# Kernel optimization log

Measured on AMD Instinct MI355X. Metric: run time of the kernel, lower is better.

The kernel has to match this reference:

```python
import jax, jax.numpy as jnp
import numpy as np

N_IN = 500000
N_OUT = 125000
K = 8          # kernel^dim = 2^3 offsets
R = 62500      # rulebook pairs per offset (strided conv: total == N_IN)
RS = 62500     # submanifold rulebook pairs per offset
C_IN = 64
C_OUT = 128
BN_EPS = 1e-4  # scn.BatchNormReLU default eps


def bn_relu(x, gamma, beta):
    # SCN BatchNormReLU in training mode: per-channel stats over active sites.
    m = jnp.mean(x, axis=0)
    v = jnp.var(x, axis=0)
    return jax.nn.relu((x - m) * jax.lax.rsqrt(v + BN_EPS) * gamma + beta)


def sparse_conv(x, W, in_idx, out_idx, n_out):
    # rulebook gather-GEMM-scatter.
    # x: [N_in, Cin]; W: [K, Cin, Cout]; in_idx/out_idx: [K, R]
    g = x[in_idx]                                   # [K, R, Cin] gather
    c = jnp.einsum('krc,kcd->krd', g, W)            # per-offset GEMM
    out = jnp.zeros((n_out, W.shape[-1]), x.dtype)
    return out.at[out_idx.reshape(-1)].add(c.reshape(-1, W.shape[-1]))


def setup_inputs() -> dict:
    key = jax.random.key(0)
    ks = jax.random.split(key, 8)
    x = jax.random.normal(ks[0], (N_IN, C_IN), dtype=jnp.float32)
    W1 = jax.random.normal(ks[1], (K, C_IN, C_OUT), dtype=jnp.float32) / np.sqrt(K * C_IN)
    Ws = jax.random.normal(ks[2], (K, C_OUT, C_OUT), dtype=jnp.float32) / np.sqrt(K * C_OUT)
    W2 = jax.random.normal(ks[3], (K, C_IN, C_OUT), dtype=jnp.float32) / np.sqrt(K * C_IN)
    in_idx1 = jax.random.randint(ks[4], (K, R), 0, N_IN, dtype=jnp.int32)
    out_idx1 = jax.random.randint(ks[5], (K, R), 0, N_OUT, dtype=jnp.int32)
    in_idx_s = jax.random.randint(ks[6], (K, RS), 0, N_OUT, dtype=jnp.int32)
    out_idx_s = jax.random.randint(ks[7], (K, RS), 0, N_OUT, dtype=jnp.int32)
    return {
        'x': x,
        'gamma1': jnp.ones((C_IN,), jnp.float32),
        'beta1': jnp.zeros((C_IN,), jnp.float32),
        'gamma2': jnp.ones((C_OUT,), jnp.float32),
        'beta2': jnp.zeros((C_OUT,), jnp.float32),
        'W1': W1, 'Ws': Ws, 'W2': W2,
        'in_idx1': in_idx1, 'out_idx1': out_idx1,
        'in_idx_s': in_idx_s, 'out_idx_s': out_idx_s,
        'n_out': N_OUT,
    }


def reference(x, gamma1, beta1, gamma2, beta2, W1, Ws, W2,
              in_idx1, out_idx1, in_idx_s, out_idx_s, n_out):
    x1 = bn_relu(x, gamma1, beta1)                              # bnr1
    y1 = sparse_conv(x1, W1, in_idx1, out_idx1, n_out)          # conv1 (stride 2)
    y1 = bn_relu(y1, gamma2, beta2)                             # bnr2
    y1 = sparse_conv(y1, Ws, in_idx_s, out_idx_s, n_out)        # submanifold conv
    y2 = sparse_conv(x1, W2, in_idx1, out_idx1, n_out)          # conv2 (same rulebook)
    return y1 + y2                                              # AddTable
```

## Files before the change

kernel.cpp:

```cpp
#include <hip/hip_runtime.h>

#define K_OFF   8
#define R_PAIRS 62500
#define NPAIRS  500000
#define N_IN    500000
#define N_OUT   125000
#define CIN     64
#define COUT    128
#define BN_EPS  1e-4f
#define NBINS_KC (N_OUT * K_OFF)
#define NB2     (2 * NBINS_KC)
#define SCAN_E2 8192
#define NSB2    245
#define BM      32
#define CHUNK   32
#define OLD_TILES 8

typedef __bf16 bf16;
typedef __bf16 bf16x4 __attribute__((ext_vector_type(4)));
typedef __bf16 bf16x8 __attribute__((ext_vector_type(8)));
typedef float  f32x4  __attribute__((ext_vector_type(4)));
typedef unsigned int u32;

__device__ __forceinline__ int zb(int row, int col_bf16) {
    int byte = (row << 10) + (col_bf16 << 1);
    return byte ^ ((row & 7) << 4);
}

template<int C>
__global__ void bn_stats_kernel(const float* __restrict__ x, int n_rows,
                                float* __restrict__ sums ) {
    constexpr int CG = C / 4;
    int tid = blockIdx.x * blockDim.x + threadIdx.x;
    int nth = gridDim.x * blockDim.x;
    const float4* x4 = (const float4*)x;
    long n4 = (long)n_rows * CG;
    int cg = tid % CG;
    float s[4] = {0,0,0,0}, q[4] = {0,0,0,0};
    for (long i = tid; i < n4; i += nth) {
        float4 v = x4[i];
        float f[4] = {v.x, v.y, v.z, v.w};
        #pragma unroll
        for (int j = 0; j < 4; j++) { s[j] += f[j]; q[j] += f[j] * f[j]; }
    }
    __shared__ float acc[2 * C];
    for (int i = threadIdx.x; i < 2 * C; i += blockDim.x) acc[i] = 0.f;
    __syncthreads();
    #pragma unroll
    for (int j = 0; j < 4; j++) {
        atomicAdd(&acc[cg * 4 + j], s[j]);
        atomicAdd(&acc[C + cg * 4 + j], q[j]);
    }
    __syncthreads();
    for (int i = threadIdx.x; i < 2 * C; i += blockDim.x) atomicAdd(&sums[i], acc[i]);
}

template<int C>
__global__ void bn_finalize_kernel(const float* __restrict__ sums,
                                   const float* __restrict__ gamma,
                                   const float* __restrict__ beta,
                                   float inv_n, float* __restrict__ ss) {
    int c = threadIdx.x;
    if (c < C) {
        float m  = sums[c] * inv_n;
        float v  = sums[C + c] * inv_n - m * m;
        float sc = gamma[c] * rsqrtf(v + BN_EPS);
        ss[c]     = sc;
        ss[C + c] = beta[c] - m * sc;
    }
}

__global__ void bn_finalize2_kernel(const float* __restrict__ S ,
                                    const float* __restrict__ gamma,
                                    const float* __restrict__ beta,
                                    float* __restrict__ ss) {
    int c = threadIdx.x;
    float s = 0.f, q = 0.f;
    for (int st = 0; st < 64; st++) { s += S[st * 256 + c]; q += S[st * 256 + 128 + c]; }
    float m = s / (float)N_OUT;
    float v = q / (float)N_OUT - m * m;
    float sc = gamma[c] * rsqrtf(v + BN_EPS);
    ss[c] = sc; ss[128 + c] = beta[c] - m * sc;
}

__global__ void pack12_kernel(const float* __restrict__ W1, const float* __restrict__ W2,
                              bf16* __restrict__ Wf) {
    int idx = blockIdx.x * 256 + threadIdx.x;
    int j = idx & 7;
    int lane = (idx >> 3) & 63;
    int fi = idx >> 9;
    int ks = fi >> 4, nfrag = fi & 15;
    int k512 = ks * 32 + (lane >> 4) * 8 + j;
    int koff = k512 >> 6, kc = k512 & 63;
    int c = nfrag * 16 + (lane & 15);
    const float* W = (c < 128) ? W1 : W2;
    Wf[idx] = (bf16)W[((long)koff * CIN + kc) * COUT + (c & 127)];
}

__global__ void packS_kernel(const float* __restrict__ Ws, bf16* __restrict__ Wf) {
    int idx = blockIdx.x * 256 + threadIdx.x;
    int j = idx & 7;
    int lane = (idx >> 3) & 63;
    int fi = idx >> 9;
    int ksg = fi >> 3, nfrag = fi & 7;
    int k1024 = ksg * 32 + (lane >> 4) * 8 + j;
    int koff = k1024 >> 7, kc = k1024 & 127;
    int c = nfrag * 16 + (lane & 15);
    Wf[idx] = (bf16)Ws[((long)koff * COUT + kc) * COUT + c];
}

__global__ void hist2_kernel(const int* __restrict__ o1, const int* __restrict__ os,
                             u32* __restrict__ counts) {
    int p = blockIdx.x * blockDim.x + threadIdx.x;
    int stride = gridDim.x * blockDim.x;
    for (; p < 2 * NPAIRS; p += stride) {
        int bin;
        if (p < NPAIRS) bin = o1[p] * K_OFF + p / R_PAIRS;
        else { int q = p - NPAIRS; bin = NBINS_KC + os[q] * K_OFF + q / R_PAIRS; }
        atomicAdd(&counts[bin], 1u);
    }
}

__global__ void scan1_kernel(const u32* __restrict__ counts, u32* __restrict__ bsum, int n) {
    __shared__ u32 sd[256];
    int tid = threadIdx.x;
    int base = blockIdx.x * SCAN_E2 + tid * 32;
    u32 s = 0;
    #pragma unroll
    for (int j = 0; j < 32; j++) { int i = base + j; if (i < n) s += counts[i]; }
    sd[tid] = s; __syncthreads();
    for (int st = 128; st > 0; st >>= 1) { if (tid < st) sd[tid] += sd[tid + st]; __syncthreads(); }
    if (tid == 0) bsum[blockIdx.x] = sd[0];
}

__global__ void scan2_kernel(u32* __restrict__ bsum, u32* __restrict__ starts, int nb, int n) {
    __shared__ u32 sd[256];
    int tid = threadIdx.x;
    u32 v = (tid < nb) ? bsum[tid] : 0;
    sd[tid] = v; __syncthreads();
    for (int st = 1; st < 256; st <<= 1) {
        u32 t = (tid >= st) ? sd[tid - st] : 0;
        __syncthreads();
        sd[tid] += t;
        __syncthreads();
    }
    if (tid < nb) bsum[tid] = sd[tid] - v;
    if (tid == 255) starts[n] = sd[255];
}

__global__ void scan3_kernel(const u32* __restrict__ counts, const u32* __restrict__ bsum,
                             u32* __restrict__ starts, int n) {
    __shared__ u32 sd[256];
    int tid = threadIdx.x;
    int base = blockIdx.x * SCAN_E2 + tid * 32;
    u32 v[32]; u32 s = 0;
    #pragma unroll
    for (int j = 0; j < 32; j++) { int i = base + j; v[j] = (i < n) ? counts[i] : 0; s += v[j]; }
    sd[tid] = s; __syncthreads();
    for (int st = 1; st < 256; st <<= 1) {
        u32 t = (tid >= st) ? sd[tid - st] : 0;
        __syncthreads();
        sd[tid] += t;
        __syncthreads();
    }
    u32 run = bsum[blockIdx.x] + sd[tid] - s;
    #pragma unroll
    for (int j = 0; j < 32; j++) { int i = base + j; if (i < n) starts[i] = run; run += v[j]; }
}

__global__ void buildF2_kernel(const int* __restrict__ i1, const int* __restrict__ o1,
                               const int* __restrict__ is, const int* __restrict__ os,
                               const u32* __restrict__ kstart, u32* __restrict__ counts,
                               u32* __restrict__ listF) {
    int p = blockIdx.x * 256 + threadIdx.x;
    if (p >= 2 * NPAIRS) return;
    int bin, in;
    if (p < NPAIRS) { bin = o1[p] * K_OFF + p / R_PAIRS; in = i1[p]; }
    else { int q = p - NPAIRS; bin = NBINS_KC + os[q] * K_OFF + q / R_PAIRS; in = is[q]; }
    u32 c = atomicSub(&counts[bin], 1u);
    listF[kstart[bin] + c - 1u] = (u32)in;
}

__global__ __launch_bounds__(512) void fused12_kernel(
    const float* __restrict__ x, const bf16* __restrict__ Wf, const float* __restrict__ ss1,
    const u32* __restrict__ kstart, const u32* __restrict__ listF,
    bf16* __restrict__ y1, bf16* __restrict__ y2b, float* __restrict__ sums2s)
{
    __shared__ bf16 z[BM * 512];
    __shared__ bf16 As[CHUNK * 64];
    __shared__ float s_sc[64], s_sh[64];
    int tid = threadIdx.x, lane = tid & 63, wave = tid >> 6;
    int o0 = blockIdx.x * BM;
    int nrow = min(BM, N_OUT - o0);
    if (tid < 64) { s_sc[tid] = ss1[tid]; s_sh[tid] = ss1[64 + tid]; }

    int row = tid >> 4, sl = tid & 15;
    int ch0 = (sl & 1) * 32;
    u32 sA = 0, eA = 0;
    if (row < nrow) {
        size_t bin = (size_t)(o0 + row) * K_OFF + (sl >> 1);
        sA = kstart[bin]; eA = kstart[bin + 1];
    }
    u32 lo  = kstart[(size_t)o0 * K_OFF];
    u32 hiS = kstart[(size_t)(o0 + nrow) * K_OFF];

    int esl  = tid >> 4;
    int cpos = (tid & 15) * 4;
    float4 pv;

    auto issue = [&](u32 base) {
        u32 idx = base + esl;
        u32 in = (idx < hiS) ? listF[idx] : 0u;
        pv = *(const float4*)(x + (size_t)in * 64 + cpos);
    };

    f32x4 a[8];
    #pragma unroll
    for (int g = 0; g < 8; g++) a[g] = (f32x4)(0.f);

    if (lo < hiS) issue(lo);
    for (u32 cb = lo; cb < hiS; cb += CHUNK) {
        int nE = (int)min((u32)CHUNK, hiS - cb);
        __syncthreads();
        if (esl < nE) {
            float f[4] = {pv.x, pv.y, pv.z, pv.w};
            bf16x4 h;
            #pragma unroll
            for (int j = 0; j < 4; j++)
                h[j] = (bf16)fmaxf(f[j] * s_sc[cpos + j] + s_sh[cpos + j], 0.f);
            *(bf16x4*)((char*)As + ((esl * 128 + cpos * 2) ^ ((esl & 7) << 4))) = h;
        }
        __syncthreads();
        if (cb + CHUNK < hiS) issue(cb + CHUNK);
        u32 pa = max(sA, cb), pb = min(eA, cb + (u32)CHUNK);
        for (u32 p = pa; p < pb; p++) {
            int slot = (int)(p - cb);
            #pragma unroll
            for (int u = 0; u < 4; u++) {
                int bo = (slot * 128 + ch0 * 2 + u * 16) ^ ((slot & 7) << 4);
                int4 vi = *(const int4*)((const char*)As + bo);
                bf16x8 hv = *(bf16x8*)&vi;
                #pragma unroll
                for (int j = 0; j < 8; j++)
                    a[u * 2 + (j >> 2)][j & 3] += (float)hv[j];
            }
        }
    }
    __syncthreads();

    {
        int colb = sl * 32;
        #pragma unroll
        for (int u = 0; u < 4; u++) {
            bf16x8 h;
            #pragma unroll
            for (int j = 0; j < 8; j++) h[j] = (bf16)a[u * 2 + (j >> 2)][j & 3];
            *(bf16x8*)((char*)z + zb(row, colb + u * 8)) = h;
        }
    }
    __syncthreads();

    int l15 = lane & 15, kr0 = (lane >> 4) * 8;
    f32x4 acc[2][2];
    #pragma unroll
    for (int m = 0; m < 2; m++)
        #pragma unroll
        for (int nf = 0; nf < 2; nf++) acc[m][nf] = (f32x4)(0.f);

    for (int ks = 0; ks < 16; ks++) {
        int colb = ks * 32 + kr0;
        bf16x8 af0 = *(bf16x8*)((char*)z + zb(l15, colb));
        bf16x8 af1 = *(bf16x8*)((char*)z + zb(l15 + 16, colb));
        #pragma unroll
        for (int nf = 0; nf < 2; nf++) {
            bf16x8 bf = *(const bf16x8*)(Wf + ((size_t)(ks * 16 + wave * 2 + nf) * 64 + lane) * 8);
            acc[0][nf] = __builtin_amdgcn_mfma_f32_16x16x32_bf16(af0, bf, acc[0][nf], 0, 0, 0);
            acc[1][nf] = __builtin_amdgcn_mfma_f32_16x16x32_bf16(af1, bf, acc[1][nf], 0, 0, 0);
        }
    }
    __syncthreads();

    bf16* st = z;
    int rb = (lane >> 4) * 4;
    #pragma unroll
    for (int m = 0; m < 2; m++)
        #pragma unroll
        for (int nf = 0; nf < 2; nf++)
            #pragma unroll
            for (int j = 0; j < 4; j++)
                st[(m * 16 + rb + j) * 256 + wave * 32 + nf * 16 + l15] = (bf16)acc[m][nf][j];
    __syncthreads();

    if (tid < 128) {
        float s = 0.f, q = 0.f;
        for (int r = 0; r < nrow; r++) { float v = (float)st[r * 256 + tid]; s += v; q += v * v; }
        int sb = (blockIdx.x & 63) * 256;
        atomicAdd(&sums2s[sb + tid], s);
        atomicAdd(&sums2s[sb + 128 + tid], q);
    }
    {
        int orow = tid >> 4, seg = tid & 15;
        if (orow < nrow) {
            const int4* src = (const int4*)(st + orow * 256 + seg * 16);
            int4 v0 = src[0], v1 = src[1];
            bf16* dst = (seg < 8) ? (y1  + (size_t)(o0 + orow) * 128 + seg * 16)
                                  : (y2b + (size_t)(o0 + orow) * 128 + (seg - 8) * 16);
            ((int4*)dst)[0] = v0; ((int4*)dst)[1] = v1;
        }
    }
}

__global__ __launch_bounds__(512) void fusedS_kernel(
    const bf16* __restrict__ y1, const bf16* __restrict__ Wf, const float* __restrict__ ss2,
    const u32* __restrict__ kstart, const u32* __restrict__ listF,
    const bf16* __restrict__ y2b, float* __restrict__ out)
{
    __shared__ bf16 z[BM * 512];
    __shared__ bf16 As[CHUNK * 128];
    __shared__ float s_sc[128], s_sh[128];
    int tid = threadIdx.x, lane = tid & 63, wave = tid >> 6;
    int o0 = blockIdx.x * BM;
    int nrow = min(BM, N_OUT - o0);
    if (tid < 128) { s_sc[tid] = ss2[tid]; s_sh[tid] = ss2[128 + tid]; }

    int row = tid >> 4, sl = tid & 15;
    int kq = sl >> 2, ch0 = (sl & 3) * 32;
    u32 sA = 0, eA = 0, sB = 0, eB = 0;
    if (row < nrow) {
        size_t binb = (size_t)(o0 + row) * K_OFF;
        sA = kstart[binb + kq];     eA = kstart[binb + kq + 1];
        sB = kstart[binb + 4 + kq]; eB = kstart[binb + 4 + kq + 1];
    }
    u32 lo  = kstart[(size_t)o0 * K_OFF];
    u32 hiS = kstart[(size_t)(o0 + nrow) * K_OFF];

    int esl  = tid >> 4;
    int cpos = (tid & 15) * 8;
    int4 pv;

    auto issue = [&](u32 base) {
        u32 idx = base + esl;
        u32 in = (idx < hiS) ? listF[idx] : 0u;
        pv = *(const int4*)(y1 + (size_t)in * 128 + cpos);
    };

    f32x4 aA[8], aB[8];
    #pragma unroll
    for (int g = 0; g < 8; g++) { aA[g] = (f32x4)(0.f); aB[g] = (f32x4)(0.f); }

    if (lo < hiS) issue(lo);
    for (u32 cb = lo; cb < hiS; cb += CHUNK) {
        int nE = (int)min((u32)CHUNK, hiS - cb);
        __syncthreads();
        if (esl < nE) {
            bf16x8 hv = *(bf16x8*)&pv;
            bf16x8 ho;
            #pragma unroll
            for (int j = 0; j < 8; j++)
                ho[j] = (bf16)fmaxf((float)hv[j] * s_sc[cpos + j] + s_sh[cpos + j], 0.f);
            *(bf16x8*)((char*)As + ((esl * 256 + cpos * 2) ^ ((esl & 7) << 4))) = ho;
        }
        __syncthreads();
        if (cb + CHUNK < hiS) issue(cb + CHUNK);
        u32 pa = max(sA, cb), pb = min(eA, cb + (u32)CHUNK);
        for (u32 p = pa; p < pb; p++) {
            int slot = (int)(p - cb);
            #pragma unroll
            for (int u = 0; u < 4; u++) {
                int bo = (slot * 256 + ch0 * 2 + u * 16) ^ ((slot & 7) << 4);
                int4 vi = *(const int4*)((const char*)As + bo);
                bf16x8 hv = *(bf16x8*)&vi;
                #pragma unroll
                for (int j = 0; j < 8; j++)
                    aA[u * 2 + (j >> 2)][j & 3] += (float)hv[j];
            }
        }
        pa = max(sB, cb); pb = min(eB, cb + (u32)CHUNK);
        for (u32 p = pa; p < pb; p++) {
            int slot = (int)(p - cb);
            #pragma unroll
            for (int u = 0; u < 4; u++) {
                int bo = (slot * 256 + ch0 * 2 + u * 16) ^ ((slot & 7) << 4);
                int4 vi = *(const int4*)((const char*)As + bo);
                bf16x8 hv = *(bf16x8*)&vi;
                #pragma unroll
                for (int j = 0; j < 8; j++)
                    aB[u * 2 + (j >> 2)][j & 3] += (float)hv[j];
            }
        }
    }

    int l15 = lane & 15, kr0 = (lane >> 4) * 8;
    f32x4 acc[2];
    acc[0] = (f32x4)(0.f); acc[1] = (f32x4)(0.f);
    int colb0 = sl * 32;

    #pragma unroll
    for (int h = 0; h < 2; h++) {
        __syncthreads();
        {
            #pragma unroll
            for (int u = 0; u < 4; u++) {
                bf16x8 hv;
                #pragma unroll
                for (int j = 0; j < 8; j++)
                    hv[j] = (bf16)((h == 0 ? aA : aB)[u * 2 + (j >> 2)][j & 3]);
                *(bf16x8*)((char*)z + zb(row, colb0 + u * 8)) = hv;
            }
        }
        __syncthreads();

        for (int ks = 0; ks < 16; ks++) {
            int colb = ks * 32 + kr0;
            bf16x8 af0 = *(bf16x8*)((char*)z + zb(l15, colb));
            bf16x8 af1 = *(bf16x8*)((char*)z + zb(l15 + 16, colb));
            int fi = (h * 16 + ks) * 8 + wave;
            bf16x8 bf = *(const bf16x8*)(Wf + ((size_t)fi * 64 + lane) * 8);
            acc[0] = __builtin_amdgcn_mfma_f32_16x16x32_bf16(af0, bf, acc[0], 0, 0, 0);
            acc[1] = __builtin_amdgcn_mfma_f32_16x16x32_bf16(af1, bf, acc[1], 0, 0, 0);
        }
    }
    __syncthreads();

    float* zf = (float*)z;
    int rb = (lane >> 4) * 4;
    #pragma unroll
    for (int m = 0; m < 2; m++)
        #pragma unroll
        for (int j = 0; j < 4; j++)
            zf[(m * 16 + rb + j) * 128 + wave * 16 + l15] = acc[m][j];
    __syncthreads();

    {
        int orow = tid >> 4, seg = tid & 15;
        if (orow < nrow) {
            f32x4 s0 = *(f32x4*)&zf[orow * 128 + seg * 8];
            f32x4 s1 = *(f32x4*)&zf[orow * 128 + seg * 8 + 4];
            int4 yv = *(const int4*)(y2b + (size_t)(o0 + orow) * 128 + seg * 8);
            bf16x8 hy = *(bf16x8*)&yv;
            float4 w0 = make_float4(s0[0] + (float)hy[0], s0[1] + (float)hy[1],
                                    s0[2] + (float)hy[2], s0[3] + (float)hy[3]);
            float4 w1 = make_float4(s1[0] + (float)hy[4], s1[1] + (float)hy[5],
                                    s1[2] + (float)hy[6], s1[3] + (float)hy[7]);
            float* dst = out + (size_t)(o0 + orow) * 128 + seg * 8;
            *(float4*)dst = w0;
            *(float4*)(dst + 4) = w1;
        }
    }
}

__global__ __launch_bounds__(256) void conv12_atomic_kernel(
    const float* __restrict__ x,
    const float* __restrict__ W1, const float* __restrict__ W2,
    const int* __restrict__ in_idx, const int* __restrict__ out_idx,
    const float* __restrict__ ss1,
    float* __restrict__ y1, float* __restrict__ y2)
{
    int k    = blockIdx.y;
    int tid  = threadIdx.x;
    int wave = tid >> 6, lane = tid & 63;

    __shared__ bf16 As[64 * 64];
    __shared__ int  s_out[64];
    __shared__ float s_sc[64], s_sh[64];
    char* asb = (char*)As;

    if (tid < 64) { s_sc[tid] = ss1[tid]; s_sh[tid] = ss1[64 + tid]; }

    const float* Wk = ((wave & 2) ? W2 : W1) + (long)k * CIN * COUT;
    int nbase = (wave & 1) * 64;
    int l15 = lane & 15;
    int kr0 = (lane >> 4) * 8;

    bf16x8 bfrag[2][4];
    #pragma unroll
    for (int ks = 0; ks < 2; ks++)
        #pragma unroll
        for (int nf = 0; nf < 4; nf++) {
            const float* p = Wk + (long)(ks * 32 + kr0) * COUT + nbase + nf * 16 + l15;
            bf16x8 b;
            #pragma unroll
            for (int j = 0; j < 8; j++) b[j] = (bf16)p[(long)j * COUT];
            bfrag[ks][nf] = b;
        }

    const int* in_k  = in_idx  + k * R_PAIRS;
    const int* out_k = out_idx + k * R_PAIRS;
    float* ybase = (wave & 2) ? y2 : y1;

    int grow = tid >> 2;
    int gcol = (tid & 3) * 16;

    __syncthreads();

    for (int t = 0; t < OLD_TILES; t++) {
        int pair0 = blockIdx.x * (OLD_TILES * 64) + t * 64;
        {
            int p = pair0 + grow;
            bool valid = p < R_PAIRS;
            long src = valid ? (long)in_k[p] : 0;
            const float4* xr = (const float4*)(x + src * CIN + gcol);
            #pragma unroll
            for (int g = 0; g < 2; g++) {
                float4 va = make_float4(0, 0, 0, 0), vb = va;
                if (valid) { va = xr[g * 2]; vb = xr[g * 2 + 1]; }
                float f[8] = {va.x, va.y, va.z, va.w, vb.x, vb.y, vb.z, vb.w};
                bf16x8 h;
                #pragma unroll
                for (int j = 0; j < 8; j++) {
                    int c = gcol + g * 8 + j;
                    h[j] = (bf16)fmaxf(f[j] * s_sc[c] + s_sh[c], 0.f);
                }
                int boff = ((grow * 128) + (gcol + g * 8) * 2) ^ ((grow & 7) << 4);
                *(bf16x8*)(asb + boff) = h;
            }
        }
        if (tid < 64) {
            int p = pair0 + tid;
            s_out[tid] = (p < R_PAIRS) ? out_k[p] : -1;
        }
        __syncthreads();

        f32x4 acc[4][4];
        #pragma unroll
        for (int m = 0; m < 4; m++)
            #pragma unroll
            for (int n = 0; n < 4; n++) acc[m][n] = (f32x4)(0.f);

        #pragma unroll
        for (int ks = 0; ks < 2; ks++) {
            bf16x8 af[4];
            #pragma unroll
            for (int m = 0; m < 4; m++) {
                int rrow = m * 16 + l15;
                int boff = (rrow * 128 + (ks * 32 + kr0) * 2) ^ ((rrow & 7) << 4);
                af[m] = *(bf16x8*)(asb + boff);
            }
            #pragma unroll
            for (int m = 0; m < 4; m++)
                #pragma unroll
                for (int nf = 0; nf < 4; nf++)
                    acc[m][nf] = __builtin_amdgcn_mfma_f32_16x16x32_bf16(
                        af[m], bfrag[ks][nf], acc[m][nf], 0, 0, 0);
        }

        int rbase = (lane >> 4) * 4;
        #pragma unroll
        for (int m = 0; m < 4; m++)
            #pragma unroll
            for (int j = 0; j < 4; j++) {
                int o = s_out[m * 16 + rbase + j];
                if (o >= 0)
                    #pragma unroll
                    for (int nf = 0; nf < 4; nf++)
                        atomicAdd(&ybase[(long)o * COUT + nbase + nf * 16 + l15],
                                  acc[m][nf][j]);
            }
        __syncthreads();
    }
}

__global__ __launch_bounds__(256) void convs_atomic_kernel(
    const float* __restrict__ y1,
    const float* __restrict__ Ws,
    const int* __restrict__ in_idx, const int* __restrict__ out_idx,
    const float* __restrict__ ss2,
    float* __restrict__ out)
{
    int k    = blockIdx.y;
    int tid  = threadIdx.x;
    int wave = tid >> 6, lane = tid & 63;

    __shared__ bf16 As[64 * 128];
    __shared__ int  s_out[64];
    __shared__ float s_sc[128], s_sh[128];
    char* asb = (char*)As;

    if (tid < 128) { s_sc[tid] = ss2[tid]; s_sh[tid] = ss2[128 + tid]; }

    const float* Wk = Ws + (long)k * COUT * COUT;
    int nbase = wave * 32;
    int l15 = lane & 15;
    int kr0 = (lane >> 4) * 8;

    bf16x8 bfrag[4][2];
    #pragma unroll
    for (int ks = 0; ks < 4; ks++)
        #pragma unroll
        for (int nf = 0; nf < 2; nf++) {
            const float* p = Wk + (long)(ks * 32 + kr0) * COUT + nbase + nf * 16 + l15;
            bf16x8 b;
            #pragma unroll
            for (int j = 0; j < 8; j++) b[j] = (bf16)p[(long)j * COUT];
            bfrag[ks][nf] = b;
        }

    const int* in_k  = in_idx  + k * R_PAIRS;
    const int* out_k = out_idx + k * R_PAIRS;

    int grow = tid >> 2;
    int gcol = (tid & 3) * 32;

    __syncthreads();

    for (int t = 0; t < OLD_TILES; t++) {
        int pair0 = blockIdx.x * (OLD_TILES * 64) + t * 64;
        {
            int p = pair0 + grow;
            bool valid = p < R_PAIRS;
            long src = valid ? (long)in_k[p] : 0;
            const float4* yr = (const float4*)(y1 + src * COUT + gcol);
            #pragma unroll
            for (int g = 0; g < 4; g++) {
                float4 va = make_float4(0, 0, 0, 0), vb = va;
                if (valid) { va = yr[g * 2]; vb = yr[g * 2 + 1]; }
                float f[8] = {va.x, va.y, va.z, va.w, vb.x, vb.y, vb.z, vb.w};
                bf16x8 h;
                #pragma unroll
                for (int j = 0; j < 8; j++) {
                    int c = gcol + g * 8 + j;
                    h[j] = (bf16)fmaxf(f[j] * s_sc[c] + s_sh[c], 0.f);
                }
                int boff = (grow * 256 + (gcol + g * 8) * 2) ^ ((grow & 7) << 4);
                *(bf16x8*)(asb + boff) = h;
            }
        }
        if (tid < 64) {
            int p = pair0 + tid;
            s_out[tid] = (p < R_PAIRS) ? out_k[p] : -1;
        }
        __syncthreads();

        f32x4 acc[4][2];
        #pragma unroll
        for (int m = 0; m < 4; m++)
            #pragma unroll
            for (int n = 0; n < 2; n++) acc[m][n] = (f32x4)(0.f);

        #pragma unroll
        for (int ks = 0; ks < 4; ks++) {
            bf16x8 af[4];
            #pragma unroll
            for (int m = 0; m < 4; m++) {
                int rrow = m * 16 + l15;
                int boff = (rrow * 256 + (ks * 32 + kr0) * 2) ^ ((rrow & 7) << 4);
                af[m] = *(bf16x8*)(asb + boff);
            }
            #pragma unroll
            for (int m = 0; m < 4; m++)
                #pragma unroll
                for (int nf = 0; nf < 2; nf++)
                    acc[m][nf] = __builtin_amdgcn_mfma_f32_16x16x32_bf16(
                        af[m], bfrag[ks][nf], acc[m][nf], 0, 0, 0);
        }

        int rbase = (lane >> 4) * 4;
        #pragma unroll
        for (int m = 0; m < 4; m++)
            #pragma unroll
            for (int j = 0; j < 4; j++) {
                int o = s_out[m * 16 + rbase + j];
                if (o >= 0)
                    #pragma unroll
                    for (int nf = 0; nf < 2; nf++)
                        atomicAdd(&out[(long)o * COUT + nbase + nf * 16 + l15],
                                  acc[m][nf][j]);
            }
        __syncthreads();
    }
}

extern "C" void kernel_launch(void* const* d_in, const int* in_sizes, int n_in,
                              void* d_out, int out_size, void* d_ws, size_t ws_size,
                              hipStream_t stream) {
    const float* x       = (const float*)d_in[0];
    const float* gamma1  = (const float*)d_in[1];
    const float* beta1   = (const float*)d_in[2];
    const float* gamma2  = (const float*)d_in[3];
    const float* beta2   = (const float*)d_in[4];
    const float* W1      = (const float*)d_in[5];
    const float* Ws      = (const float*)d_in[6];
    const float* W2      = (const float*)d_in[7];
    const int*   in_idx1   = (const int*)d_in[8];
    const int*   out_idx1  = (const int*)d_in[9];
    const int*   in_idx_s  = (const int*)d_in[10];
    const int*   out_idx_s = (const int*)d_in[11];

    float* out = (float*)d_out;
    char*  ws  = (char*)d_ws;

    auto a256 = [](size_t v) { return (v + 255) & ~(size_t)255; };

    size_t off_y1      = 0;
    size_t off_y2b     = a256(off_y1 + 32000000);
    size_t off_stats   = a256(off_y2b + 32000000);
    size_t off_s2s     = a256(off_stats + 4096);
    size_t off_counts  = a256(off_s2s + 65536);
    size_t off_kstart  = a256(off_counts + 4ull * NB2);
    size_t off_bsum    = a256(off_kstart + 4ull * (NB2 + 1));
    size_t off_list    = a256(off_bsum + 1024);
    size_t off_wf12    = a256(off_list + 4ull * 2 * NPAIRS);
    size_t off_wfs     = a256(off_wf12 + 262144);
    size_t need        = off_wfs + 262144;

    if (need > ws_size) {
        float* y1f   = (float*)ws;
        float* stats = y1f + (long)N_OUT * COUT;
        float* sums1 = stats;
        float* ss1   = stats + 128;
        float* sums2 = stats + 256;
        float* ss2   = stats + 512;

        hipMemsetAsync(d_out, 0, (size_t)N_OUT * COUT * 4, stream);
        hipMemsetAsync(d_ws,  0, (size_t)N_OUT * COUT * 4 + 768 * 4, stream);

        bn_stats_kernel<64><<<1024, 256, 0, stream>>>(x, N_IN, sums1);
        bn_finalize_kernel<64><<<1, 64, 0, stream>>>(sums1, gamma1, beta1, 1.f / N_IN, ss1);

        dim3 cgrid((R_PAIRS + OLD_TILES * 64 - 1) / (OLD_TILES * 64), K_OFF);
        conv12_atomic_kernel<<<cgrid, 256, 0, stream>>>(x, W1, W2, in_idx1, out_idx1, ss1, y1f, out);

        bn_stats_kernel<128><<<1024, 256, 0, stream>>>(y1f, N_OUT, sums2);
        bn_finalize_kernel<128><<<1, 128, 0, stream>>>(sums2, gamma2, beta2, 1.f / N_OUT, ss2);

        convs_atomic_kernel<<<cgrid, 256, 0, stream>>>(y1f, Ws, in_idx_s, out_idx_s, ss2, out);
        return;
    }

    bf16*  y1      = (bf16*)(ws + off_y1);
    bf16*  y2b     = (bf16*)(ws + off_y2b);
    float* sums1   = (float*)(ws + off_stats);
    float* ss1     = sums1 + 256;
    float* ss2     = sums1 + 512;
    float* s2s     = (float*)(ws + off_s2s);
    u32*   counts  = (u32*)(ws + off_counts);
    u32*   kstart  = (u32*)(ws + off_kstart);
    u32*   bsum    = (u32*)(ws + off_bsum);
    u32*   list    = (u32*)(ws + off_list);
    bf16*  wf12    = (bf16*)(ws + off_wf12);
    bf16*  wfs     = (bf16*)(ws + off_wfs);

    int nblk = (N_OUT + BM - 1) / BM;

    hipMemsetAsync(ws + off_stats, 0, off_counts - off_stats, stream);
    hipMemsetAsync(counts, 0, 4ull * NB2, stream);

    hist2_kernel<<<1024, 256, 0, stream>>>(out_idx1, out_idx_s, counts);
    scan1_kernel<<<NSB2, 256, 0, stream>>>(counts, bsum, NB2);
    scan2_kernel<<<1, 256, 0, stream>>>(bsum, kstart, NSB2, NB2);
    scan3_kernel<<<NSB2, 256, 0, stream>>>(counts, bsum, kstart, NB2);
    buildF2_kernel<<<(2 * NPAIRS + 255) / 256, 256, 0, stream>>>(
        in_idx1, out_idx1, in_idx_s, out_idx_s, kstart, counts, list);

    bn_stats_kernel<64><<<1024, 256, 0, stream>>>(x, N_IN, sums1);
    bn_finalize_kernel<64><<<1, 64, 0, stream>>>(sums1, gamma1, beta1, 1.f / N_IN, ss1);
    pack12_kernel<<<512, 256, 0, stream>>>(W1, W2, wf12);
    packS_kernel<<<512, 256, 0, stream>>>(Ws, wfs);

    fused12_kernel<<<nblk, 512, 0, stream>>>(x, wf12, ss1, kstart, list, y1, y2b, s2s);
    bn_finalize2_kernel<<<1, 128, 0, stream>>>(s2s, gamma2, beta2, ss2);

    fusedS_kernel<<<nblk, 512, 0, stream>>>(y1, wfs, ss2, kstart + NBINS_KC, list, y2b, out);
}
```

Baseline: 384.3 us.

## Bucket rulebook by output row only and pack offset into list entries

The counting sort now builds bins per output row instead of per (row, offset), which shrinks the histogram and scan arrays by a factor of eight. The kernel offset is packed into the top byte of each list entry, stored in shared memory per chunk, and each thread filters slots by its offset. This removes the large scans over 2M bins, which should cut counts and prefix-sum traffic. In exchange every thread now walks all entries of its row and branches on a metadata check, which adds wasted iterations and divergence in the accumulation loops.

After: 540.2 us. +40.6%, slower.

```diff
diff --git a/kernel.cpp b/kernel.cpp
--- a/kernel.cpp
+++ b/kernel.cpp
@@ -8,10 +8,9 @@
 #define CIN     64
 #define COUT    128
 #define BN_EPS  1e-4f
-#define NBINS_KC (N_OUT * K_OFF)
-#define NB2     (2 * NBINS_KC)
-#define SCAN_E2 8192
-#define NSB2    245
+#define NB2     (2 * N_OUT)
+#define SCAN_E  1024
+#define NSB     245
 #define BM      32
 #define CHUNK   32
 #define OLD_TILES 8
@@ -114,9 +113,7 @@
     int p = blockIdx.x * blockDim.x + threadIdx.x;
     int stride = gridDim.x * blockDim.x;
     for (; p < 2 * NPAIRS; p += stride) {
-        int bin;
-        if (p < NPAIRS) bin = o1[p] * K_OFF + p / R_PAIRS;
-        else { int q = p - NPAIRS; bin = NBINS_KC + os[q] * K_OFF + q / R_PAIRS; }
+        int bin = (p < NPAIRS) ? o1[p] : (N_OUT + os[p - NPAIRS]);
         atomicAdd(&counts[bin], 1u);
     }
 }
@@ -124,10 +121,10 @@
 __global__ void scan1_kernel(const u32* __restrict__ counts, u32* __restrict__ bsum, int n) {
     __shared__ u32 sd[256];
     int tid = threadIdx.x;
-    int base = blockIdx.x * SCAN_E2 + tid * 32;
+    int base = blockIdx.x * SCAN_E + tid * 4;
     u32 s = 0;
     #pragma unroll
-    for (int j = 0; j < 32; j++) { int i = base + j; if (i < n) s += counts[i]; }
+    for (int j = 0; j < 4; j++) { int i = base + j; if (i < n) s += counts[i]; }
     sd[tid] = s; __syncthreads();
     for (int st = 128; st > 0; st >>= 1) { if (tid < st) sd[tid] += sd[tid + st]; __syncthreads(); }
     if (tid == 0) bsum[blockIdx.x] = sd[0];
@@ -152,10 +149,10 @@
                              u32* __restrict__ starts, int n) {
     __shared__ u32 sd[256];
     int tid = threadIdx.x;
-    int base = blockIdx.x * SCAN_E2 + tid * 32;
-    u32 v[32]; u32 s = 0;
-    #pragma unroll
-    for (int j = 0; j < 32; j++) { int i = base + j; v[j] = (i < n) ? counts[i] : 0; s += v[j]; }
+    int base = blockIdx.x * SCAN_E + tid * 4;
+    u32 v[4]; u32 s = 0;
+    #pragma unroll
+    for (int j = 0; j < 4; j++) { int i = base + j; v[j] = (i < n) ? counts[i] : 0; s += v[j]; }
     sd[tid] = s; __syncthreads();
     for (int st = 1; st < 256; st <<= 1) {
         u32 t = (tid >= st) ? sd[tid - st] : 0;
@@ -165,29 +162,36 @@
     }
     u32 run = bsum[blockIdx.x] + sd[tid] - s;
     #pragma unroll
-    for (int j = 0; j < 32; j++) { int i = base + j; if (i < n) starts[i] = run; run += v[j]; }
+    for (int j = 0; j < 4; j++) { int i = base + j; if (i < n) starts[i] = run; run += v[j]; }
 }
 
 __global__ void buildF2_kernel(const int* __restrict__ i1, const int* __restrict__ o1,
                                const int* __restrict__ is, const int* __restrict__ os,
-                               const u32* __restrict__ kstart, u32* __restrict__ counts,
+                               const u32* __restrict__ rowstart, u32* __restrict__ counts,
                                u32* __restrict__ listF) {
     int p = blockIdx.x * 256 + threadIdx.x;
     if (p >= 2 * NPAIRS) return;
-    int bin, in;
-    if (p < NPAIRS) { bin = o1[p] * K_OFF + p / R_PAIRS; in = i1[p]; }
-    else { int q = p - NPAIRS; bin = NBINS_KC + os[q] * K_OFF + q / R_PAIRS; in = is[q]; }
+    int bin; u32 w;
+    if (p < NPAIRS) {
+        bin = o1[p];
+        w = (u32)i1[p] | ((u32)(p / R_PAIRS) << 24);
+    } else {
+        int q = p - NPAIRS;
+        bin = N_OUT + os[q];
+        w = (u32)is[q] | ((u32)(q / R_PAIRS) << 24);
+    }
     u32 c = atomicSub(&counts[bin], 1u);
-    listF[kstart[bin] + c - 1u] = (u32)in;
+    listF[rowstart[bin] + c - 1u] = w;
 }
 
 __global__ __launch_bounds__(512) void fused12_kernel(
     const float* __restrict__ x, const bf16* __restrict__ Wf, const float* __restrict__ ss1,
-    const u32* __restrict__ kstart, const u32* __restrict__ listF,
+    const u32* __restrict__ rowstart, const u32* __restrict__ listF,
     bf16* __restrict__ y1, bf16* __restrict__ y2b, float* __restrict__ sums2s)
 {
     __shared__ bf16 z[BM * 512];
     __shared__ bf16 As[CHUNK * 64];
+    __shared__ u32 s_meta[CHUNK];
     __shared__ float s_sc[64], s_sh[64];
     int tid = threadIdx.x, lane = tid & 63, wave = tid >> 6;
     int o0 = blockIdx.x * BM;
@@ -195,23 +199,20 @@
     if (tid < 64) { s_sc[tid] = ss1[tid]; s_sh[tid] = ss1[64 + tid]; }
 
     int row = tid >> 4, sl = tid & 15;
-    int ch0 = (sl & 1) * 32;
-    u32 sA = 0, eA = 0;
-    if (row < nrow) {
-        size_t bin = (size_t)(o0 + row) * K_OFF + (sl >> 1);
-        sA = kstart[bin]; eA = kstart[bin + 1];
-    }
-    u32 lo  = kstart[(size_t)o0 * K_OFF];
-    u32 hiS = kstart[(size_t)(o0 + nrow) * K_OFF];
+    int kown = sl >> 1, ch0 = (sl & 1) * 32;
+    u32 rs = 0, re = 0;
+    if (row < nrow) { rs = rowstart[o0 + row]; re = rowstart[o0 + row + 1]; }
+    u32 lo  = rowstart[o0];
+    u32 hiS = rowstart[o0 + nrow];
 
     int esl  = tid >> 4;
     int cpos = (tid & 15) * 4;
-    float4 pv;
+    u32 pw; float4 pv;
 
     auto issue = [&](u32 base) {
         u32 idx = base + esl;
-        u32 in = (idx < hiS) ? listF[idx] : 0u;
-        pv = *(const float4*)(x + (size_t)in * 64 + cpos);
+        pw = (idx < hiS) ? listF[idx] : 0u;
+        pv = *(const float4*)(x + (size_t)(pw & 0xFFFFFF) * 64 + cpos);
     };
 
     f32x4 a[8];
@@ -229,12 +230,14 @@
             for (int j = 0; j < 4; j++)
                 h[j] = (bf16)fmaxf(f[j] * s_sc[cpos + j] + s_sh[cpos + j], 0.f);
             *(bf16x4*)((char*)As + ((esl * 128 + cpos * 2) ^ ((esl & 7) << 4))) = h;
+            if ((tid & 15) == 0) s_meta[esl] = pw >> 24;
         }
         __syncthreads();
         if (cb + CHUNK < hiS) issue(cb + CHUNK);
-        u32 pa = max(sA, cb), pb = min(eA, cb + (u32)CHUNK);
+        u32 pa = max(rs, cb), pb = min(re, cb + (u32)CHUNK);
         for (u32 p = pa; p < pb; p++) {
             int slot = (int)(p - cb);
+            if ((int)s_meta[slot] != kown) continue;
             #pragma unroll
             for (int u = 0; u < 4; u++) {
                 int bo = (slot * 128 + ch0 * 2 + u * 16) ^ ((slot & 7) << 4);
@@ -312,11 +315,12 @@
 
 __global__ __launch_bounds__(512) void fusedS_kernel(
     const bf16* __restrict__ y1, const bf16* __restrict__ Wf, const float* __restrict__ ss2,
-    const u32* __restrict__ kstart, const u32* __restrict__ listF,
+    const u32* __restrict__ rowstart, const u32* __restrict__ listF,
     const bf16* __restrict__ y2b, float* __restrict__ out)
 {
     __shared__ bf16 z[BM * 512];
     __shared__ bf16 As[CHUNK * 128];
+    __shared__ u32 s_meta[CHUNK];
     __shared__ float s_sc[128], s_sh[128];
     int tid = threadIdx.x, lane = tid & 63, wave = tid >> 6;
     int o0 = blockIdx.x * BM;
@@ -325,23 +329,19 @@
 
     int row = tid >> 4, sl = tid & 15;
     int kq = sl >> 2, ch0 = (sl & 3) * 32;
-    u32 sA = 0, eA = 0, sB = 0, eB = 0;
-    if (row < nrow) {
-        size_t binb = (size_t)(o0 + row) * K_OFF;
-        sA = kstart[binb + kq];     eA = kstart[binb + kq + 1];
-        sB = kstart[binb + 4 + kq]; eB = kstart[binb + 4 + kq + 1];
-    }
-    u32 lo  = kstart[(size_t)o0 * K_OFF];
-    u32 hiS = kstart[(size_t)(o0 + nrow) * K_OFF];
+    u32 rs = 0, re = 0;
+    if (row < nrow) { rs = rowstart[o0 + row]; re = rowstart[o0 + row + 1]; }
+    u32 lo  = rowstart[o0];
+    u32 hiS = rowstart[o0 + nrow];
 
     int esl  = tid >> 4;
     int cpos = (tid & 15) * 8;
-    int4 pv;
+    u32 pw; int4 pv;
 
     auto issue = [&](u32 base) {
         u32 idx = base + esl;
-        u32 in = (idx < hiS) ? listF[idx] : 0u;
-        pv = *(const int4*)(y1 + (size_t)in * 128 + cpos);
+        pw = (idx < hiS) ? listF[idx] : 0u;
+        pv = *(const int4*)(y1 + (size_t)(pw & 0xFFFFFF) * 128 + cpos);
     };
 
     f32x4 aA[8], aB[8];
@@ -359,12 +359,16 @@
             for (int j = 0; j < 8; j++)
                 ho[j] = (bf16)fmaxf((float)hv[j] * s_sc[cpos + j] + s_sh[cpos + j], 0.f);
             *(bf16x8*)((char*)As + ((esl * 256 + cpos * 2) ^ ((esl & 7) << 4))) = ho;
+            if ((tid & 15) == 0) s_meta[esl] = pw >> 24;
         }
         __syncthreads();
         if (cb + CHUNK < hiS) issue(cb + CHUNK);
-        u32 pa = max(sA, cb), pb = min(eA, cb + (u32)CHUNK);
+        u32 pa = max(rs, cb), pb = min(re, cb + (u32)CHUNK);
         for (u32 p = pa; p < pb; p++) {
             int slot = (int)(p - cb);
+            int k = (int)s_meta[slot];
+            if ((k & 3) != kq) continue;
+            f32x4 t[8];
             #pragma unroll
             for (int u = 0; u < 4; u++) {
                 int bo = (slot * 256 + ch0 * 2 + u * 16) ^ ((slot & 7) << 4);
@@ -372,20 +376,14 @@
                 bf16x8 hv = *(bf16x8*)&vi;
                 #pragma unroll
                 for (int j = 0; j < 8; j++)
-                    aA[u * 2 + (j >> 2)][j & 3] += (float)hv[j];
-            }
-        }
-        pa = max(sB, cb); pb = min(eB, cb + (u32)CHUNK);
-        for (u32 p = pa; p < pb; p++) {
-            int slot = (int)(p - cb);
-            #pragma unroll
-            for (int u = 0; u < 4; u++) {
-                int bo = (slot * 256 + ch0 * 2 + u * 16) ^ ((slot & 7) << 4);
-                int4 vi = *(const int4*)((const char*)As + bo);
-                bf16x8 hv = *(bf16x8*)&vi;
-                #pragma unroll
-                for (int j = 0; j < 8; j++)
-                    aB[u * 2 + (j >> 2)][j & 3] += (float)hv[j];
+                    t[u * 2 + (j >> 2)][j & 3] = (float)hv[j];
+            }
+            if (k < 4) {
+                #pragma unroll
+                for (int g = 0; g < 8; g++) aA[g] += t[g];
+            } else {
+                #pragma unroll
+                for (int g = 0; g < 8; g++) aB[g] += t[g];
             }
         }
     }
@@ -441,7 +439,9 @@
             float4 w0 = make_float4(s0[0] + (float)hy[0], s0[1] + (float)hy[1],
                                     s0[2] + (float)hy[2], s0[3] + (float)hy[3]);
             float4 w1 = make_float4(s1[0] + (float)hy[4], s1[1] + (float)hy[5],
-                                    s1[2] + (float)hy[6], s1[3] + (float)hy[7]);
+                                    s1[2] + (float)hy[6], s1[7 - 7] + 0.f);
+            w1 = make_float4(s1[0] + (float)hy[4], s1[1] + (float)hy[5],
+                             s1[2] + (float)hy[6], s1[3] + (float)hy[7]);
             float* dst = out + (size_t)(o0 + orow) * 128 + seg * 8;
             *(float4*)dst = w0;
             *(float4*)(dst + 4) = w1;
@@ -696,8 +696,8 @@
     size_t off_stats   = a256(off_y2b + 32000000);
     size_t off_s2s     = a256(off_stats + 4096);
     size_t off_counts  = a256(off_s2s + 65536);
-    size_t off_kstart  = a256(off_counts + 4ull * NB2);
-    size_t off_bsum    = a256(off_kstart + 4ull * (NB2 + 1));
+    size_t off_rows    = a256(off_counts + 4ull * NB2);
+    size_t off_bsum    = a256(off_rows + 4ull * (NB2 + 1));
     size_t off_list    = a256(off_bsum + 1024);
     size_t off_wf12    = a256(off_list + 4ull * 2 * NPAIRS);
     size_t off_wfs     = a256(off_wf12 + 262144);
@@ -734,7 +734,7 @@
     float* ss2     = sums1 + 512;
     float* s2s     = (float*)(ws + off_s2s);
     u32*   counts  = (u32*)(ws + off_counts);
-    u32*   kstart  = (u32*)(ws + off_kstart);
+    u32*   rowst   = (u32*)(ws + off_rows);
     u32*   bsum    = (u32*)(ws + off_bsum);
     u32*   list    = (u32*)(ws + off_list);
     bf16*  wf12    = (bf16*)(ws + off_wf12);
@@ -746,19 +746,19 @@
     hipMemsetAsync(counts, 0, 4ull * NB2, stream);
 
     hist2_kernel<<<1024, 256, 0, stream>>>(out_idx1, out_idx_s, counts);
-    scan1_kernel<<<NSB2, 256, 0, stream>>>(counts, bsum, NB2);
-    scan2_kernel<<<1, 256, 0, stream>>>(bsum, kstart, NSB2, NB2);
-    scan3_kernel<<<NSB2, 256, 0, stream>>>(counts, bsum, kstart, NB2);
+    scan1_kernel<<<NSB, 256, 0, stream>>>(counts, bsum, NB2);
+    scan2_kernel<<<1, 256, 0, stream>>>(bsum, rowst, NSB, NB2);
+    scan3_kernel<<<NSB, 256, 0, stream>>>(counts, bsum, rowst, NB2);
     buildF2_kernel<<<(2 * NPAIRS + 255) / 256, 256, 0, stream>>>(
-        in_idx1, out_idx1, in_idx_s, out_idx_s, kstart, counts, list);
+        in_idx1, out_idx1, in_idx_s, out_idx_s, rowst, counts, list);
 
     bn_stats_kernel<64><<<1024, 256, 0, stream>>>(x, N_IN, sums1);
     bn_finalize_kernel<64><<<1, 64, 0, stream>>>(sums1, gamma1, beta1, 1.f / N_IN, ss1);
     pack12_kernel<<<512, 256, 0, stream>>>(W1, W2, wf12);
     packS_kernel<<<512, 256, 0, stream>>>(Ws, wfs);
 
-    fused12_kernel<<<nblk, 512, 0, stream>>>(x, wf12, ss1, kstart, list, y1, y2b, s2s);
+    fused12_kernel<<<nblk, 512, 0, stream>>>(x, wf12, ss1, rowst, list, y1, y2b, s2s);
     bn_finalize2_kernel<<<1, 128, 0, stream>>>(s2s, gamma2, beta2, ss2);
 
-    fusedS_kernel<<<nblk, 512, 0, stream>>>(y1, wfs, ss2, kstart + NBINS_KC, list, y2b, out);
-}
+    fusedS_kernel<<<nblk, 512, 0, stream>>>(y1, wfs, ss2, rowst + N_OUT, list, y2b, out);
+}
```

## Deepen gather prefetch to two chunks and double-buffer LDS in fusedS

Applied to the files above, without the earlier changes.

Both gather loops now prefetch the rulebook index two chunks ahead and the feature row one chunk ahead. The next feature load is issued before the barrier instead of after it, so it overlaps the accumulation phase. In the submanifold kernel the LDS staging buffer is doubled, which removes one barrier per chunk. This hides gather latency at the cost of more registers and LDS, and the index is masked to 24 bits.

Result: faster. 370.5 us (-3.6%).

```diff
diff --git a/kernel.cpp b/kernel.cpp
--- a/kernel.cpp
+++ b/kernel.cpp
@@ -206,19 +206,20 @@
 
     int esl  = tid >> 4;
     int cpos = (tid & 15) * 4;
-    float4 pv;
-
-    auto issue = [&](u32 base) {
-        u32 idx = base + esl;
-        u32 in = (idx < hiS) ? listF[idx] : 0u;
-        pv = *(const float4*)(x + (size_t)in * 64 + cpos);
-    };
+    u32 pwN; float4 pv;
+
+    {
+        u32 i0 = lo + esl;
+        u32 w = (i0 < hiS) ? listF[i0] : 0u;
+        pv = *(const float4*)(x + (size_t)w * 64 + cpos);
+        u32 i1 = lo + CHUNK + esl;
+        pwN = (i1 < hiS) ? listF[i1] : 0u;
+    }
 
     f32x4 a[8];
     #pragma unroll
     for (int g = 0; g < 8; g++) a[g] = (f32x4)(0.f);
 
-    if (lo < hiS) issue(lo);
     for (u32 cb = lo; cb < hiS; cb += CHUNK) {
         int nE = (int)min((u32)CHUNK, hiS - cb);
         __syncthreads();
@@ -230,8 +231,10 @@
                 h[j] = (bf16)fmaxf(f[j] * s_sc[cpos + j] + s_sh[cpos + j], 0.f);
             *(bf16x4*)((char*)As + ((esl * 128 + cpos * 2) ^ ((esl & 7) << 4))) = h;
         }
-        __syncthreads();
-        if (cb + CHUNK < hiS) issue(cb + CHUNK);
+        float4 pvN = *(const float4*)(x + (size_t)(pwN & 0xFFFFFFu) * 64 + cpos);
+        u32 i2 = cb + 2 * CHUNK + esl;
+        u32 pwNN = (i2 < hiS) ? listF[i2] : 0u;
+        __syncthreads();
         u32 pa = max(sA, cb), pb = min(eA, cb + (u32)CHUNK);
         for (u32 p = pa; p < pb; p++) {
             int slot = (int)(p - cb);
@@ -245,6 +248,7 @@
                     a[u * 2 + (j >> 2)][j & 3] += (float)hv[j];
             }
         }
+        pv = pvN; pwN = pwNN;
     }
     __syncthreads();
 
@@ -316,7 +320,7 @@
     const bf16* __restrict__ y2b, float* __restrict__ out)
 {
     __shared__ bf16 z[BM * 512];
-    __shared__ bf16 As[CHUNK * 128];
+    __shared__ bf16 As[2][CHUNK * 128];
     __shared__ float s_sc[128], s_sh[128];
     int tid = threadIdx.x, lane = tid & 63, wave = tid >> 6;
     int o0 = blockIdx.x * BM;
@@ -336,39 +340,44 @@
 
     int esl  = tid >> 4;
     int cpos = (tid & 15) * 8;
-    int4 pv;
-
-    auto issue = [&](u32 base) {
-        u32 idx = base + esl;
-        u32 in = (idx < hiS) ? listF[idx] : 0u;
-        pv = *(const int4*)(y1 + (size_t)in * 128 + cpos);
-    };
+    u32 pwN; int4 pv;
+
+    {
+        u32 i0 = lo + esl;
+        u32 w = (i0 < hiS) ? listF[i0] : 0u;
+        pv = *(const int4*)(y1 + (size_t)w * 128 + cpos);
+        u32 i1 = lo + CHUNK + esl;
+        pwN = (i1 < hiS) ? listF[i1] : 0u;
+    }
 
     f32x4 aA[8], aB[8];
     #pragma unroll
     for (int g = 0; g < 8; g++) { aA[g] = (f32x4)(0.f); aB[g] = (f32x4)(0.f); }
 
-    if (lo < hiS) issue(lo);
-    for (u32 cb = lo; cb < hiS; cb += CHUNK) {
+    __syncthreads();
+
+    int ci = 0;
+    for (u32 cb = lo; cb < hiS; cb += CHUNK, ci ^= 1) {
         int nE = (int)min((u32)CHUNK, hiS - cb);
-        __syncthreads();
         if (esl < nE) {
             bf16x8 hv = *(bf16x8*)&pv;
             bf16x8 ho;
             #pragma unroll
             for (int j = 0; j < 8; j++)
                 ho[j] = (bf16)fmaxf((float)hv[j] * s_sc[cpos + j] + s_sh[cpos + j], 0.f);
-            *(bf16x8*)((char*)As + ((esl * 256 + cpos * 2) ^ ((esl & 7) << 4))) = ho;
-        }
-        __syncthreads();
-        if (cb + CHUNK < hiS) issue(cb + CHUNK);
+            *(bf16x8*)((char*)As[ci] + ((esl * 256 + cpos * 2) ^ ((esl & 7) << 4))) = ho;
+        }
+        int4 pvN = *(const int4*)(y1 + (size_t)(pwN & 0xFFFFFFu) * 128 + cpos);
+        u32 i2 = cb + 2 * CHUNK + esl;
+        u32 pwNN = (i2 < hiS) ? listF[i2] : 0u;
+        __syncthreads();
         u32 pa = max(sA, cb), pb = min(eA, cb + (u32)CHUNK);
         for (u32 p = pa; p < pb; p++) {
             int slot = (int)(p - cb);
             #pragma unroll
             for (int u = 0; u < 4; u++) {
                 int bo = (slot * 256 + ch0 * 2 + u * 16) ^ ((slot & 7) << 4);
-                int4 vi = *(const int4*)((const char*)As + bo);
+                int4 vi = *(const int4*)((const char*)As[ci] + bo);
                 bf16x8 hv = *(bf16x8*)&vi;
                 #pragma unroll
                 for (int j = 0; j < 8; j++)
@@ -381,13 +390,14 @@
             #pragma unroll
             for (int u = 0; u < 4; u++) {
                 int bo = (slot * 256 + ch0 * 2 + u * 16) ^ ((slot & 7) << 4);
-                int4 vi = *(const int4*)((const char*)As + bo);
+                int4 vi = *(const int4*)((const char*)As[ci] + bo);
                 bf16x8 hv = *(bf16x8*)&vi;
                 #pragma unroll
                 for (int j = 0; j < 8; j++)
                     aB[u * 2 + (j >> 2)][j & 3] += (float)hv[j];
             }
         }
+        pv = pvN; pwN = pwNN;
     }
 
     int l15 = lane & 15, kr0 = (lane >> 4) * 8;
```
